# Kernel tuning notes

Measured on AMD Instinct MI355X. Metric: run time of the kernel, lower is better.

## Reference

```python
import jax, jax.numpy as jnp
import numpy as np

B, T, V, E, H, L = 32, 128, 32000, 256, 256, 2


def setup_inputs() -> dict:
    key = jax.random.key(0)
    ks = jax.random.split(key, 9)
    s = 0.05  # weight scale to keep gates out of deep saturation
    x = jax.random.randint(ks[0], (B, T), 0, V, dtype=jnp.int32)
    return {
        "x": x,
        "embed_table": jax.random.normal(ks[1], (V, E), jnp.float32) * 0.1,
        "fW": jax.random.normal(ks[2], (L, E, 4 * H), jnp.float32) * s,
        "fU": jax.random.normal(ks[3], (L, H, 4 * H), jnp.float32) * s,
        "fb": jnp.zeros((L, 4 * H), jnp.float32),
        "bW": jax.random.normal(ks[4], (L, E, 4 * H), jnp.float32) * s,
        "bU": jax.random.normal(ks[5], (L, H, 4 * H), jnp.float32) * s,
        "bb": jnp.zeros((L, 4 * H), jnp.float32),
        "Wp": jax.random.normal(ks[6], (2 * H, V), jnp.float32) * s,
        "bp": jnp.zeros((V,), jnp.float32),
        "Wn": jax.random.normal(ks[7], ((T - 2) * 2 * H, 2), jnp.float32) * s,
        "bn": jnp.zeros((2,), jnp.float32),
    }


def run_stacked_lstm(emb, mask, W, U, b):
    """emb: [B,S,D], mask: [B,S] bool. Keras LSTMCell gate order (i,f,g,o);
    masked steps carry state through (output = previous top-layer h)."""
    nL = W.shape[0]
    Bz = emb.shape[0]
    Hd = U.shape[1]
    emb_t = jnp.swapaxes(emb, 0, 1)   # [S,B,D]
    mask_t = jnp.swapaxes(mask, 0, 1)  # [S,B]
    h0 = jnp.zeros((nL, Bz, Hd), emb.dtype)

    def step(carry, inp):
        hs, cs = carry
        x_t, m_t = inp
        m = m_t[:, None]
        new_h, new_c = [], []
        inp_x = x_t
        for l in range(nL):
            z = inp_x @ W[l] + hs[l] @ U[l] + b[l]
            i, f, g, o = jnp.split(z, 4, axis=-1)
            c = jax.nn.sigmoid(f) * cs[l] + jax.nn.sigmoid(i) * jnp.tanh(g)
            h = jax.nn.sigmoid(o) * jnp.tanh(c)
            h = jnp.where(m, h, hs[l])
            c = jnp.where(m, c, cs[l])
            new_h.append(h)
            new_c.append(c)
            inp_x = h
        return (jnp.stack(new_h), jnp.stack(new_c)), inp_x

    _, ys = jax.lax.scan(step, (h0, h0), (emb_t, mask_t))
    return jnp.swapaxes(ys, 0, 1)  # [B,S,H]


def reference(x, embed_table, fW, fU, fb, bW, bU, bb, Wp, bp, Wn, bn):
    o = embed_table[x]            # [B,T,E]
    mask = x != 0                 # mask_zero=True
    # forward LSTM over tokens 0..T-2
    f = run_stacked_lstm(o[:, :-1], mask[:, :-1], fW, fU, fb)
    # backward LSTM (go_backwards=True): run over reversed o[:,1:];
    # Keras RNN leaves outputs in reversed-time order.
    b_out = run_stacked_lstm(o[:, 1:][:, ::-1], mask[:, 1:][:, ::-1], bW, bU, bb)
    ctx = jnp.concatenate([f[:, :-1], b_out[:, 1:]], axis=-1)  # [B,T-2,2H]
    word_logits = ctx @ Wp + bp                                 # [B,T-2,V]
    nsp_logits = ctx.reshape(ctx.shape[0], -1) @ Wn + bn        # [B,2]
    return word_logits, nsp_logits
```

## Files before the change

### kernel.cpp

```cpp
#include <hip/hip_runtime.h>
#include <stdint.h>

typedef __bf16 bf16;
typedef __bf16 bf16x8 __attribute__((ext_vector_type(8)));
typedef float  f32x4  __attribute__((ext_vector_type(4)));

#define NB 16
#define OFF_CTR    0
#define CTR_BYTES  (4*128*4)
#define OFF_HIST   2048
#define HIST_ONE   (128*32*256*2)
#define OFF_H0F    (OFF_HIST)
#define OFF_H0B    (OFF_HIST + 1*HIST_ONE)
#define OFF_H1F    (OFF_HIST + 2*HIST_ONE)
#define OFF_H1B    (OFF_HIST + 3*HIST_ONE)
#define OFF_XF     (OFF_HIST + 4*HIST_ONE)
#define XF_BYTES   (4064*256*2)
#define OFF_XB     (OFF_XF + XF_BYTES)
#define OFF_FW0T   (OFF_XB + XF_BYTES)
#define W0T_BYTES  (1024*256*2)
#define OFF_BW0T   (OFF_FW0T + W0T_BYTES)
#define OFF_PRE0F  (OFF_BW0T + W0T_BYTES)
#define PRE_BYTES  (4064*1024*4)
#define OFF_PRE0B  (OFF_PRE0F + PRE_BYTES)
#define OFF_WPT    (OFF_PRE0B + PRE_BYTES)
#define WPT_BYTES  (32000*512*2)
#define OFF_CTX    (OFF_WPT + WPT_BYTES)
#define CTX_BYTES  (4032*512*2)
#define OFF_MF     (OFF_CTX + CTX_BYTES)
#define OFF_MB     (OFF_MF + 4096)
#define ZERO_BYTES OFF_XF

__device__ __forceinline__ int swz8(int row, int kblk) { return (kblk ^ (row & 7)) << 3; }

__device__ __forceinline__ uint64_t sys_load_u64(const uint64_t* p) {
  return __hip_atomic_load(p, __ATOMIC_RELAXED, __HIP_MEMORY_SCOPE_SYSTEM);
}
__device__ __forceinline__ void sys_store_u16(unsigned short* p, unsigned short v) {
  __hip_atomic_store(p, v, __ATOMIC_RELAXED, __HIP_MEMORY_SCOPE_SYSTEM);
}

__global__ __launch_bounds__(256) void embed_kernel(
    const int* __restrict__ x, const float* __restrict__ tab,
    bf16* __restrict__ xf, bf16* __restrict__ xb,
    unsigned char* __restrict__ mf, unsigned char* __restrict__ mb)
{
  int t = blockIdx.x;
  int b = blockIdx.y;
  int k = threadIdx.x;
  int tokf = x[b*128 + t];
  int tokb = x[b*128 + 127 - t];
  xf[(size_t)(t*32+b)*256 + k] = (bf16)tab[(size_t)tokf*256 + k];
  xb[(size_t)(t*32+b)*256 + k] = (bf16)tab[(size_t)tokb*256 + k];
  if (k == 0) { mf[t*32+b] = (tokf != 0); mb[t*32+b] = (tokb != 0); }
}

__global__ __launch_bounds__(256) void transpose_to_bf16(
    const float* __restrict__ in, bf16* __restrict__ out, int R, int C)
{
  __shared__ float tile[64][65];
  int c0 = blockIdx.x*64, r0 = blockIdx.y*64;
  int tid = threadIdx.x;
  int r = tid >> 2, cs = (tid & 3)*16;
  #pragma unroll
  for (int i = 0; i < 16; i += 4) {
    float4 v = *(const float4*)(in + (size_t)(r0+r)*C + c0 + cs + i);
    tile[r][cs+i+0]=v.x; tile[r][cs+i+1]=v.y; tile[r][cs+i+2]=v.z; tile[r][cs+i+3]=v.w;
  }
  __syncthreads();
  int c = tid >> 2, rs = (tid & 3)*16;
  #pragma unroll
  for (int i = 0; i < 16; ++i)
    out[(size_t)(c0+c)*R + r0 + rs + i] = (bf16)tile[rs+i][c];
}

__global__ __launch_bounds__(256) void gemm_bf16(
    const bf16* __restrict__ A, const bf16* __restrict__ BT,
    const float* __restrict__ bias, float* __restrict__ C,
    int M, int N, int K)
{
  __shared__ bf16 As[128][72];
  __shared__ bf16 Bs[128][72];
  int tid = threadIdx.x;
  int row0 = blockIdx.x*128, col0 = blockIdx.y*128;
  int wave = tid >> 6, lane = tid & 63, l15 = lane & 15, quad = lane >> 4;
  int wm = (wave & 1)*64, wn = (wave >> 1)*64;
  f32x4 acc[4][4] = {};
  for (int kk = 0; kk < K; kk += 64) {
    #pragma unroll
    for (int i = 0; i < 4; ++i) {
      int o = i*256 + tid;
      int r = o >> 3, seg = o & 7;
      int gr = row0 + r;
      if (gr < M) *(uint4*)&As[r][seg*8] = *(const uint4*)(A + (size_t)gr*K + kk + seg*8);
      else        *(uint4*)&As[r][seg*8] = make_uint4(0,0,0,0);
      *(uint4*)&Bs[r][seg*8] = *(const uint4*)(BT + (size_t)(col0 + r)*K + kk + seg*8);
    }
    __syncthreads();
    #pragma unroll
    for (int ks = 0; ks < 64; ks += 32) {
      bf16x8 af[4], bfr[4];
      #pragma unroll
      for (int mi = 0; mi < 4; ++mi) af[mi]  = *(const bf16x8*)&As[wm + mi*16 + l15][ks + quad*8];
      #pragma unroll
      for (int ni = 0; ni < 4; ++ni) bfr[ni] = *(const bf16x8*)&Bs[wn + ni*16 + l15][ks + quad*8];
      #pragma unroll
      for (int mi = 0; mi < 4; ++mi)
        #pragma unroll
        for (int ni = 0; ni < 4; ++ni)
          acc[mi][ni] = __builtin_amdgcn_mfma_f32_16x16x32_bf16(af[mi], bfr[ni], acc[mi][ni], 0, 0, 0);
    }
    __syncthreads();
  }
  #pragma unroll
  for (int ni = 0; ni < 4; ++ni) {
    int col = col0 + wn + ni*16 + l15;
    float bv = bias[col];
    #pragma unroll
    for (int mi = 0; mi < 4; ++mi) {
      int rbase = row0 + wm + mi*16 + quad*4;
      #pragma unroll
      for (int r = 0; r < 4; ++r) {
        int grow = rbase + r;
        if (grow < M) C[(size_t)grow*N + col] = acc[mi][ni][r] + bv;
      }
    }
  }
}

__global__ __launch_bounds__(512) void recur_kernel(
    const float* __restrict__ pre0f, const float* __restrict__ pre0b,
    const float* __restrict__ fU0, const float* __restrict__ bU0,
    const float* __restrict__ fW1, const float* __restrict__ fU1,
    const float* __restrict__ bW1, const float* __restrict__ bU1,
    const float* __restrict__ fb1, const float* __restrict__ bb1,
    const unsigned char* __restrict__ mf, const unsigned char* __restrict__ mb,
    bf16* __restrict__ h0f, bf16* __restrict__ h0b,
    bf16* __restrict__ h1f, bf16* __restrict__ h1b,
    int* __restrict__ ctr)
{
  __shared__ bf16 U_T[64][512];
  __shared__ bf16 hA[32][512];
  float (*z_s)[65] = (float (*)[65])hA;

  int tid = threadIdx.x;
  int bx = blockIdx.x;
  int dir = bx >> 5, stage = (bx >> 4) & 1, blk = bx & 15;
  int j0 = blk * 16;
  const float* pre = dir ? pre0b : pre0f;
  const unsigned char* mgl = dir ? mb : mf;
  bf16* h0 = dir ? h0b : h0f;
  bf16* h1 = dir ? h1b : h1f;
  const int K = stage ? 512 : 256;
  int* c0 = ctr + (dir*2 + 0)*128;
  int* c1 = ctr + (dir*2 + 1)*128;

  if (stage == 0) {
    const float* U = dir ? bU0 : fU0;
    for (int idx = tid; idx < 64*256; idx += 512) {
      int k = idx >> 6, c = idx & 63;
      int gc = (c >> 4)*256 + j0 + (c & 15);
      U_T[c][swz8(c, k >> 3) | (k & 7)] = (bf16)U[(size_t)k*1024 + gc];
    }
  } else {
    const float* W = dir ? bW1 : fW1;
    const float* U = dir ? bU1 : fU1;
    for (int idx = tid; idx < 64*512; idx += 512) {
      int k = idx >> 6, c = idx & 63;
      int gc = (c >> 4)*256 + j0 + (c & 15);
      float v = (k < 256) ? W[(size_t)k*1024 + gc] : U[(size_t)(k-256)*1024 + gc];
      U_T[c][swz8(c, k >> 3) | (k & 7)] = (bf16)v;
    }
  }
  int gb = tid & 31, gu = tid >> 5;
  float c_state = 0.f, h_state = 0.f;
  float bi = 0.f, bff = 0.f, bgg = 0.f, boo = 0.f;
  if (stage == 1) {
    const float* bias = dir ? bb1 : fb1;
    bi  = bias[0*256 + j0 + gu];
    bff = bias[1*256 + j0 + gu];
    bgg = bias[2*256 + j0 + gu];
    boo = bias[3*256 + j0 + gu];
  }
  int wave = tid >> 6, lane = tid & 63, l15 = lane & 15, quad = lane >> 4;
  int m0 = (wave & 1)*16, n0 = (wave >> 1)*16;
  __syncthreads();

  for (int t = 0; t < 127; ++t) {
    float p_i = bi, p_f = bff, p_g = bgg, p_o = boo;
    if (stage == 0) {
      const float* p = pre + ((size_t)t*32 + gb)*1024 + j0 + gu;
      p_i = p[0]; p_f = p[256]; p_g = p[512]; p_o = p[768];
    }
    unsigned char msk = mgl[t*32 + gb];

    if (tid == 0) {
      int spins;
      if (stage == 0) {
        if (t > 0) { spins = 0;
          while (__hip_atomic_load(&c0[t-1], __ATOMIC_RELAXED, __HIP_MEMORY_SCOPE_SYSTEM) < NB)
            { if (++spins > 4096) __builtin_amdgcn_s_sleep(1); if (spins > (1<<18)) break; } }
      } else {
        spins = 0;
        while (__hip_atomic_load(&c0[t], __ATOMIC_RELAXED, __HIP_MEMORY_SCOPE_SYSTEM) < NB)
          { if (++spins > 4096) __builtin_amdgcn_s_sleep(1); if (spins > (1<<18)) break; }
        if (t > 0) { spins = 0;
          while (__hip_atomic_load(&c1[t-1], __ATOMIC_RELAXED, __HIP_MEMORY_SCOPE_SYSTEM) < NB)
            { if (++spins > 4096) __builtin_amdgcn_s_sleep(1); if (spins > (1<<18)) break; } }
      }
      __atomic_signal_fence(__ATOMIC_SEQ_CST);
    }
    __syncthreads();

    if (stage == 0) {
      const uint64_t* src = (const uint64_t*)(h0 + (size_t)t*8192);
      #pragma unroll
      for (int i = 0; i < 4; ++i) {
        int q = i*512 + tid;
        int r = q >> 6, seg = q & 63;
        uint64_t v = sys_load_u64(src + q);
        *(uint64_t*)&hA[r][swz8(r, seg >> 1) + (seg & 1)*4] = v;
      }
    } else {
      const uint64_t* s0p = (const uint64_t*)(h0 + (size_t)(t+1)*8192);
      const uint64_t* s1p = (const uint64_t*)(h1 + (size_t)t*8192);
      #pragma unroll
      for (int i = 0; i < 8; ++i) {
        int q = i*512 + tid;
        int sel = q >> 11;
        int r = (q >> 6) & 31, seg = q & 63;
        const uint64_t* sp = sel ? s1p : s0p;
        uint64_t v = sys_load_u64(sp + r*64 + seg);
        int oct = (seg >> 1) + sel*32;
        *(uint64_t*)&hA[r][swz8(r, oct) + (seg & 1)*4] = v;
      }
    }
    __syncthreads();

    f32x4 acc = {0.f, 0.f, 0.f, 0.f};
    for (int kc = 0; kc < K; kc += 32) {
      int kb = (kc >> 3) + quad;
      bf16x8 a  = *(const bf16x8*)&hA[m0 + l15][swz8(m0 + l15, kb)];
      bf16x8 bb = *(const bf16x8*)&U_T[n0 + l15][swz8(n0 + l15, kb)];
      acc = __builtin_amdgcn_mfma_f32_16x16x32_bf16(a, bb, acc, 0, 0, 0);
    }
    __syncthreads();
    #pragma unroll
    for (int r = 0; r < 4; ++r) z_s[m0 + quad*4 + r][n0 + l15] = acc[r];
    __syncthreads();

    float zi = z_s[gb][ 0 + gu] + p_i;
    float zf = z_s[gb][16 + gu] + p_f;
    float zg = z_s[gb][32 + gu] + p_g;
    float zo = z_s[gb][48 + gu] + p_o;
    float ig = 1.f/(1.f + expf(-zi));
    float fg = 1.f/(1.f + expf(-zf));
    float gg = tanhf(zg);
    float og = 1.f/(1.f + expf(-zo));
    float cn = fg*c_state + ig*gg;
    float hn = og*tanhf(cn);
    if (msk) { c_state = cn; h_state = hn; }

    bf16 hv = (bf16)h_state;
    unsigned short hb;
    __builtin_memcpy(&hb, &hv, 2);
    unsigned short* dst = (unsigned short*)((stage == 0 ? h0 : h1) + (size_t)(t+1)*8192 + gb*256 + j0 + gu);
    sys_store_u16(dst, hb);
    asm volatile("s_waitcnt vmcnt(0)" ::: "memory");
    __syncthreads();
    if (tid == 0) {
      __atomic_signal_fence(__ATOMIC_SEQ_CST);
      __hip_atomic_fetch_add(stage == 0 ? &c0[t] : &c1[t], 1, __ATOMIC_RELAXED, __HIP_MEMORY_SCOPE_SYSTEM);
    }
    __syncthreads();
  }
}

__global__ __launch_bounds__(256) void ctx_kernel(
    const bf16* __restrict__ h1f, const bf16* __restrict__ h1b, bf16* __restrict__ ctx)
{
  int tau = blockIdx.x;
  int b = blockIdx.y;
  int k = threadIdx.x;
  size_t r = (size_t)(b*126 + tau)*512;
  ctx[r + k]       = h1f[(size_t)(tau+1)*8192 + b*256 + k];
  ctx[r + 256 + k] = h1b[(size_t)(tau+2)*8192 + b*256 + k];
}

__global__ __launch_bounds__(256) void nsp_kernel(
    const bf16* __restrict__ ctx, const float* __restrict__ Wn,
    const float* __restrict__ bn, float* __restrict__ out)
{
  int b = blockIdx.x, tid = threadIdx.x;
  const unsigned short* cb = (const unsigned short*)ctx;
  float a0 = 0.f, a1 = 0.f;
  for (int flat = tid; flat < 64512; flat += 256) {
    int tau = flat >> 9, k = flat & 511;
    float cv = __uint_as_float((unsigned)cb[(size_t)(b*126 + tau)*512 + k] << 16);
    float2 w = *(const float2*)(Wn + 2*(size_t)flat);
    a0 += cv*w.x; a1 += cv*w.y;
  }
  __shared__ float r0[256], r1[256];
  r0[tid] = a0; r1[tid] = a1;
  __syncthreads();
  for (int s = 128; s > 0; s >>= 1) {
    if (tid < s) { r0[tid] += r0[tid+s]; r1[tid] += r1[tid+s]; }
    __syncthreads();
  }
  if (tid == 0) { out[b*2+0] = r0[0] + bn[0]; out[b*2+1] = r1[0] + bn[1]; }
}

extern "C" void kernel_launch(void* const* d_in, const int* in_sizes, int n_in,
                              void* d_out, int out_size, void* d_ws, size_t ws_size,
                              hipStream_t stream)
{
  const int*   x   = (const int*)d_in[0];
  const float* tab = (const float*)d_in[1];
  const float* fW  = (const float*)d_in[2];
  const float* fU  = (const float*)d_in[3];
  const float* fb  = (const float*)d_in[4];
  const float* bW  = (const float*)d_in[5];
  const float* bU  = (const float*)d_in[6];
  const float* bb  = (const float*)d_in[7];
  const float* Wp  = (const float*)d_in[8];
  const float* bp  = (const float*)d_in[9];
  const float* Wn  = (const float*)d_in[10];
  const float* bn  = (const float*)d_in[11];
  float* out = (float*)d_out;
  char* ws = (char*)d_ws;

  int*  ctr   = (int*)(ws + OFF_CTR);
  bf16* h0f   = (bf16*)(ws + OFF_H0F);
  bf16* h0b   = (bf16*)(ws + OFF_H0B);
  bf16* h1f   = (bf16*)(ws + OFF_H1F);
  bf16* h1b   = (bf16*)(ws + OFF_H1B);
  bf16* xf    = (bf16*)(ws + OFF_XF);
  bf16* xb    = (bf16*)(ws + OFF_XB);
  bf16* fW0T  = (bf16*)(ws + OFF_FW0T);
  bf16* bW0T  = (bf16*)(ws + OFF_BW0T);
  float* pre0f = (float*)(ws + OFF_PRE0F);
  float* pre0b = (float*)(ws + OFF_PRE0B);
  bf16* WpT   = (bf16*)(ws + OFF_WPT);
  bf16* ctx   = (bf16*)(ws + OFF_CTX);
  unsigned char* mf = (unsigned char*)(ws + OFF_MF);
  unsigned char* mb = (unsigned char*)(ws + OFF_MB);

  hipMemsetAsync(ws, 0, ZERO_BYTES, stream);

  embed_kernel<<<dim3(127, 32), 256, 0, stream>>>(x, tab, xf, xb, mf, mb);

  transpose_to_bf16<<<dim3(16, 4),  256, 0, stream>>>(fW, fW0T, 256, 1024);
  transpose_to_bf16<<<dim3(16, 4),  256, 0, stream>>>(bW, bW0T, 256, 1024);
  transpose_to_bf16<<<dim3(500, 8), 256, 0, stream>>>(Wp, WpT, 512, 32000);

  gemm_bf16<<<dim3(32, 8), 256, 0, stream>>>(xf, fW0T, fb, pre0f, 4064, 1024, 256);
  gemm_bf16<<<dim3(32, 8), 256, 0, stream>>>(xb, bW0T, bb, pre0b, 4064, 1024, 256);

  recur_kernel<<<64, 512, 0, stream>>>(
      pre0f, pre0b,
      fU, bU,
      fW + 262144, fU + 262144, bW + 262144, bU + 262144,
      fb + 1024, bb + 1024,
      mf, mb, h0f, h0b, h1f, h1b, ctr);

  ctx_kernel<<<dim3(126, 32), 256, 0, stream>>>(h1f, h1b, ctx);

  gemm_bf16<<<dim3(32, 250), 256, 0, stream>>>(ctx, WpT, bp, out, 4032, 32000, 512);

  nsp_kernel<<<32, 256, 0, stream>>>(ctx, Wn, bn, out + (size_t)4032*32000);
}
```

Measured before the change: 1.718 ms.

## Use per-block step flags, split layer-1 matmul, async GEMM loads, smaller memset

The recurrent kernel replaces per-step atomic counters with per-block monotonic flags. Sixteen threads poll them in parallel instead of thread 0 spinning on a counter, and the trailing barrier after signalling is dropped. Layer 1 now starts its input-projection MFMAs on the layer-0 hidden state before it waits on its own previous hidden state, so that wait overlaps compute. The GEMM switches to global_load_lds direct-to-LDS loads with unpadded tiles, which may add bank conflicts. The workspace memset is shrunk to only the counters and the initial hidden-state slots.

```diff
diff --git a/kernel.cpp b/kernel.cpp
--- a/kernel.cpp
+++ b/kernel.cpp
@@ -29,7 +29,6 @@
 #define CTX_BYTES  (4032*512*2)
 #define OFF_MF     (OFF_CTX + CTX_BYTES)
 #define OFF_MB     (OFF_MF + 4096)
-#define ZERO_BYTES OFF_XF
 
 __device__ __forceinline__ int swz8(int row, int kblk) { return (kblk ^ (row & 7)) << 3; }
 
@@ -38,6 +37,30 @@
 }
 __device__ __forceinline__ void sys_store_u16(unsigned short* p, unsigned short v) {
   __hip_atomic_store(p, v, __ATOMIC_RELAXED, __HIP_MEMORY_SCOPE_SYSTEM);
+}
+__device__ __forceinline__ int sys_load_i32(const int* p) {
+  return __hip_atomic_load(p, __ATOMIC_RELAXED, __HIP_MEMORY_SCOPE_SYSTEM);
+}
+__device__ __forceinline__ void sys_store_i32(int* p, int v) {
+  __hip_atomic_store(p, v, __ATOMIC_RELAXED, __HIP_MEMORY_SCOPE_SYSTEM);
+}
+
+__device__ __forceinline__ void wait_flags(const int* f, int want, int tid) {
+  if (tid < NB) {
+    int spins = 0;
+    while (sys_load_i32(&f[tid]) < want) {
+      if (++spins > (1<<16)) __builtin_amdgcn_s_sleep(2);
+      if (spins > (1<<20)) break;
+    }
+  }
+  __atomic_signal_fence(__ATOMIC_SEQ_CST);
+  __syncthreads();
+}
+
+typedef __attribute__((address_space(1))) unsigned int as1_u32;
+typedef __attribute__((address_space(3))) unsigned int as3_u32;
+__device__ __forceinline__ void gload16(const void* g, void* l) {
+  __builtin_amdgcn_global_load_lds((as1_u32*)g, (as3_u32*)l, 16, 0, 0);
 }
 
 __global__ __launch_bounds__(256) void embed_kernel(
@@ -79,22 +102,22 @@
     const float* __restrict__ bias, float* __restrict__ C,
     int M, int N, int K)
 {
-  __shared__ bf16 As[128][72];
-  __shared__ bf16 Bs[128][72];
+  __shared__ bf16 As[128][64];
+  __shared__ bf16 Bs[128][64];
   int tid = threadIdx.x;
   int row0 = blockIdx.x*128, col0 = blockIdx.y*128;
   int wave = tid >> 6, lane = tid & 63, l15 = lane & 15, quad = lane >> 4;
   int wm = (wave & 1)*64, wn = (wave >> 1)*64;
+  int lr = lane >> 3;
+  int lc = (lane & 7)*8;
   f32x4 acc[4][4] = {};
   for (int kk = 0; kk < K; kk += 64) {
     #pragma unroll
     for (int i = 0; i < 4; ++i) {
-      int o = i*256 + tid;
-      int r = o >> 3, seg = o & 7;
-      int gr = row0 + r;
-      if (gr < M) *(uint4*)&As[r][seg*8] = *(const uint4*)(A + (size_t)gr*K + kk + seg*8);
-      else        *(uint4*)&As[r][seg*8] = make_uint4(0,0,0,0);
-      *(uint4*)&Bs[r][seg*8] = *(const uint4*)(BT + (size_t)(col0 + r)*K + kk + seg*8);
+      int rb = (wave*4 + i)*8;
+      int ga = row0 + rb + lr; if (ga > M-1) ga = M-1;
+      gload16(A  + (size_t)ga*K + kk + lc,                 &As[rb][0]);
+      gload16(BT + (size_t)(col0 + rb + lr)*K + kk + lc,   &Bs[rb][0]);
     }
     __syncthreads();
     #pragma unroll
@@ -141,7 +164,7 @@
 {
   __shared__ bf16 U_T[64][512];
   __shared__ bf16 hA[32][512];
-  float (*z_s)[65] = (float (*)[65])hA;
+  __shared__ float z_s[32][65];
 
   int tid = threadIdx.x;
   int bx = blockIdx.x;
@@ -151,9 +174,8 @@
   const unsigned char* mgl = dir ? mb : mf;
   bf16* h0 = dir ? h0b : h0f;
   bf16* h1 = dir ? h1b : h1f;
-  const int K = stage ? 512 : 256;
-  int* c0 = ctr + (dir*2 + 0)*128;
-  int* c1 = ctr + (dir*2 + 1)*128;
+  int* f0 = ctr + (dir*2 + 0)*16;
+  int* f1 = ctr + (dir*2 + 1)*16;
 
   if (stage == 0) {
     const float* U = dir ? bU0 : fU0;
@@ -193,26 +215,10 @@
       p_i = p[0]; p_f = p[256]; p_g = p[512]; p_o = p[768];
     }
     unsigned char msk = mgl[t*32 + gb];
-
-    if (tid == 0) {
-      int spins;
-      if (stage == 0) {
-        if (t > 0) { spins = 0;
-          while (__hip_atomic_load(&c0[t-1], __ATOMIC_RELAXED, __HIP_MEMORY_SCOPE_SYSTEM) < NB)
-            { if (++spins > 4096) __builtin_amdgcn_s_sleep(1); if (spins > (1<<18)) break; } }
-      } else {
-        spins = 0;
-        while (__hip_atomic_load(&c0[t], __ATOMIC_RELAXED, __HIP_MEMORY_SCOPE_SYSTEM) < NB)
-          { if (++spins > 4096) __builtin_amdgcn_s_sleep(1); if (spins > (1<<18)) break; }
-        if (t > 0) { spins = 0;
-          while (__hip_atomic_load(&c1[t-1], __ATOMIC_RELAXED, __HIP_MEMORY_SCOPE_SYSTEM) < NB)
-            { if (++spins > 4096) __builtin_amdgcn_s_sleep(1); if (spins > (1<<18)) break; } }
-      }
-      __atomic_signal_fence(__ATOMIC_SEQ_CST);
-    }
-    __syncthreads();
+    f32x4 acc = {0.f, 0.f, 0.f, 0.f};
 
     if (stage == 0) {
+      if (t > 0) wait_flags(f0, t, tid);
       const uint64_t* src = (const uint64_t*)(h0 + (size_t)t*8192);
       #pragma unroll
       for (int i = 0; i < 4; ++i) {
@@ -221,30 +227,48 @@
         uint64_t v = sys_load_u64(src + q);
         *(uint64_t*)&hA[r][swz8(r, seg >> 1) + (seg & 1)*4] = v;
       }
+      __syncthreads();
+      for (int kc = 0; kc < 256; kc += 32) {
+        int kb = (kc >> 3) + quad;
+        bf16x8 a = *(const bf16x8*)&hA[m0 + l15][swz8(m0 + l15, kb)];
+        bf16x8 w = *(const bf16x8*)&U_T[n0 + l15][swz8(n0 + l15, kb)];
+        acc = __builtin_amdgcn_mfma_f32_16x16x32_bf16(a, w, acc, 0, 0, 0);
+      }
     } else {
+      wait_flags(f0, t+1, tid);
       const uint64_t* s0p = (const uint64_t*)(h0 + (size_t)(t+1)*8192);
+      #pragma unroll
+      for (int i = 0; i < 4; ++i) {
+        int q = i*512 + tid;
+        int r = q >> 6, seg = q & 63;
+        uint64_t v = sys_load_u64(s0p + q);
+        *(uint64_t*)&hA[r][swz8(r, seg >> 1) + (seg & 1)*4] = v;
+      }
+      __syncthreads();
+      for (int kc = 0; kc < 256; kc += 32) {
+        int kb = (kc >> 3) + quad;
+        bf16x8 a = *(const bf16x8*)&hA[m0 + l15][swz8(m0 + l15, kb)];
+        bf16x8 w = *(const bf16x8*)&U_T[n0 + l15][swz8(n0 + l15, kb)];
+        acc = __builtin_amdgcn_mfma_f32_16x16x32_bf16(a, w, acc, 0, 0, 0);
+      }
+      if (t > 0) wait_flags(f1, t, tid);
       const uint64_t* s1p = (const uint64_t*)(h1 + (size_t)t*8192);
       #pragma unroll
-      for (int i = 0; i < 8; ++i) {
+      for (int i = 0; i < 4; ++i) {
         int q = i*512 + tid;
-        int sel = q >> 11;
-        int r = (q >> 6) & 31, seg = q & 63;
-        const uint64_t* sp = sel ? s1p : s0p;
-        uint64_t v = sys_load_u64(sp + r*64 + seg);
-        int oct = (seg >> 1) + sel*32;
-        *(uint64_t*)&hA[r][swz8(r, oct) + (seg & 1)*4] = v;
-      }
-    }
-    __syncthreads();
-
-    f32x4 acc = {0.f, 0.f, 0.f, 0.f};
-    for (int kc = 0; kc < K; kc += 32) {
-      int kb = (kc >> 3) + quad;
-      bf16x8 a  = *(const bf16x8*)&hA[m0 + l15][swz8(m0 + l15, kb)];
-      bf16x8 bb = *(const bf16x8*)&U_T[n0 + l15][swz8(n0 + l15, kb)];
-      acc = __builtin_amdgcn_mfma_f32_16x16x32_bf16(a, bb, acc, 0, 0, 0);
-    }
-    __syncthreads();
+        int r = q >> 6, seg = q & 63;
+        uint64_t v = sys_load_u64(s1p + q);
+        *(uint64_t*)&hA[r][swz8(r, (seg >> 1) + 32) + (seg & 1)*4] = v;
+      }
+      __syncthreads();
+      for (int kc = 256; kc < 512; kc += 32) {
+        int kb = (kc >> 3) + quad;
+        bf16x8 a = *(const bf16x8*)&hA[m0 + l15][swz8(m0 + l15, kb)];
+        bf16x8 w = *(const bf16x8*)&U_T[n0 + l15][swz8(n0 + l15, kb)];
+        acc = __builtin_amdgcn_mfma_f32_16x16x32_bf16(a, w, acc, 0, 0, 0);
+      }
+    }
+
     #pragma unroll
     for (int r = 0; r < 4; ++r) z_s[m0 + quad*4 + r][n0 + l15] = acc[r];
     __syncthreads();
@@ -270,9 +294,8 @@
     __syncthreads();
     if (tid == 0) {
       __atomic_signal_fence(__ATOMIC_SEQ_CST);
-      __hip_atomic_fetch_add(stage == 0 ? &c0[t] : &c1[t], 1, __ATOMIC_RELAXED, __HIP_MEMORY_SCOPE_SYSTEM);
-    }
-    __syncthreads();
+      sys_store_i32(stage == 0 ? &f0[blk] : &f1[blk], t+1);
+    }
   }
 }
 
@@ -345,7 +368,11 @@
   unsigned char* mf = (unsigned char*)(ws + OFF_MF);
   unsigned char* mb = (unsigned char*)(ws + OFF_MB);
 
-  hipMemsetAsync(ws, 0, ZERO_BYTES, stream);
+  hipMemsetAsync(ws + OFF_CTR, 0, CTR_BYTES, stream);
+  hipMemsetAsync(ws + OFF_H0F, 0, 16384, stream);
+  hipMemsetAsync(ws + OFF_H0B, 0, 16384, stream);
+  hipMemsetAsync(ws + OFF_H1F, 0, 16384, stream);
+  hipMemsetAsync(ws + OFF_H1B, 0, 16384, stream);
 
   embed_kernel<<<dim3(127, 32), 256, 0, stream>>>(x, tab, xf, xb, mf, mb);
 
```

Result: faster. 1.677 ms (-2.4%).
